# Kernel tuning notes

Measured on AMD Instinct MI355X. Metric: run time of the kernel, lower is better.

Reference implementation:

```python
import jax, jax.numpy as jnp
import numpy as np

B, S, D, H = 2, 2048, 1024, 16
HD = D // H  # head dim = 64


def setup_inputs() -> dict:
    key0 = jax.random.key(0)
    ks = jax.random.split(key0, 12)
    scale = 1.0 / np.sqrt(D)
    inp = {
        "query": jax.random.normal(ks[0], (B, S, D), jnp.float32),
        "key": jax.random.normal(ks[1], (B, S, D), jnp.float32),
        "value": jax.random.normal(ks[2], (B, S, D), jnp.float32),
        "mask": jax.random.randint(ks[3], (B, S), 0, 2, jnp.int32),
        "Wq": jax.random.normal(ks[4], (D, D), jnp.float32) * scale,
        "bq": jnp.zeros((D,), jnp.float32),
        "Wk": jax.random.normal(ks[5], (D, D), jnp.float32) * scale,
        "bk": jnp.zeros((D,), jnp.float32),
        "Wv": jax.random.normal(ks[6], (D, D), jnp.float32) * scale,
        "bv": jnp.zeros((D,), jnp.float32),
        "Wo": jax.random.normal(ks[7], (D, D), jnp.float32) * scale,
        "bo": jnp.zeros((D,), jnp.float32),
    }
    return inp


def _split_heads(x):  # (B,S,D) -> (B,H,S,HD)
    Bb, Ss, Dd = x.shape
    return x.reshape(Bb, Ss, H, HD).transpose(0, 2, 1, 3)


def reference(query, key, value, mask, Wq, bq, Wk, bk, Wv, bv, Wo, bo):
    # Linear projections (torch Linear: x @ W.T + b), split into heads.
    q = _split_heads(query @ Wq.T + bq)
    k = _split_heads(key @ Wk.T + bk)
    v = _split_heads(value @ Wv.T + bv)
    # Scaled dot-product scores: (B,H,S,S); NOTE: original divides by sqrt(head_dim).
    scores = jnp.einsum("bhqd,bhkd->bhqk", q, k) / np.sqrt(HD).astype(np.float32)
    # mask (B,S) masks KEY positions; broadcast over heads and query positions.
    scores = jnp.where(mask[:, None, None, :] == 0, jnp.float32(-1e9), scores)
    attn = jax.nn.softmax(scores, axis=-1)
    # Dropout is identity in eval mode.
    x = jnp.einsum("bhqk,bhkd->bhqd", attn, v)  # (B,H,S,HD)
    x = x.transpose(0, 2, 1, 3).reshape(query.shape[0], query.shape[1], D)
    return x @ Wo.T + bo
```

## Files before the change

### kernel.cpp

```cpp
#include <hip/hip_runtime.h>
#include <hip/hip_bf16.h>
#include <hip/hip_fp16.h>

#define BB 2
#define SS 2048
#define DD 1024
#define HH 16
#define HD 64
#define MM (BB * SS)

typedef __attribute__((ext_vector_type(8))) _Float16 half8;
typedef __attribute__((ext_vector_type(4))) float f32x4;
typedef __attribute__((ext_vector_type(4))) short short4v;

static __device__ __forceinline__ short f2h(float f) {
    _Float16 h = (_Float16)f;
    return __builtin_bit_cast(short, h);
}

static __device__ __forceinline__ unsigned pk2(float a, float b) {
    auto h = __builtin_amdgcn_cvt_pkrtz(a, b);
    return __builtin_bit_cast(unsigned, h);
}

static __device__ __forceinline__ float fexp2(float x) {
    return __builtin_amdgcn_exp2f(x);
}

static __device__ __forceinline__ void gload16(const void* g, void* l) {
    __builtin_amdgcn_global_load_lds(
        (const __attribute__((address_space(1))) unsigned*)g,
        (__attribute__((address_space(3))) unsigned*)l, 16, 0, 0);
}

__global__ __launch_bounds__(256) void cvt_kernel(
    const float* __restrict__ wq, const float* __restrict__ wk,
    const float* __restrict__ wv, const float* __restrict__ wo,
    const int* __restrict__ mask,
    short* __restrict__ wq16, short* __restrict__ wk16,
    short* __restrict__ wv16, short* __restrict__ wo16,
    float* __restrict__ mbias)
{
    const int i = (blockIdx.x * 256 + threadIdx.x) * 4;
    if (blockIdx.y == 4) {
        if (i >= BB * SS) return;
        const int4 mi = *(const int4*)&mask[i];
        float4 f;
        f.x = (mi.x == 0) ? -1.0e9f : 0.0f;
        f.y = (mi.y == 0) ? -1.0e9f : 0.0f;
        f.z = (mi.z == 0) ? -1.0e9f : 0.0f;
        f.w = (mi.w == 0) ? -1.0e9f : 0.0f;
        *(float4*)&mbias[i] = f;
        return;
    }
    const float* src; short* dst;
    switch (blockIdx.y) {
        case 0: src = wq; dst = wq16; break;
        case 1: src = wk; dst = wk16; break;
        case 2: src = wv; dst = wv16; break;
        default: src = wo; dst = wo16; break;
    }
    if (i >= DD * DD) return;
    const float4 f = *(const float4*)&src[i];
    short4v h;
    h.x = f2h(f.x); h.y = f2h(f.y); h.z = f2h(f.z); h.w = f2h(f.w);
    *(short4v*)&dst[i] = h;
}

template<bool AFP32>
__global__ __launch_bounds__(256) void gemm_f16(
    const void* __restrict__ A0, const void* __restrict__ A1, const void* __restrict__ A2,
    const short* __restrict__ W0, const short* __restrict__ W1, const short* __restrict__ W2,
    const float* __restrict__ b0, const float* __restrict__ b1, const float* __restrict__ b2,
    void* __restrict__ C0, void* __restrict__ C1, void* __restrict__ C2,
    int mode0, int mode1, int mode2)
{
    constexpr int TM = 64;
    constexpr int WN = 32;
    constexpr int NI = 2;

    const int z = blockIdx.z;
    const void* A = (z == 0) ? A0 : (z == 1) ? A1 : A2;
    const short* W = (z == 0) ? W0 : (z == 1) ? W1 : W2;
    const float* bias = (z == 0) ? b0 : (z == 1) ? b1 : b2;
    void* C = (z == 0) ? C0 : (z == 1) ? C1 : C2;
    const int mode = (z == 0) ? mode0 : (z == 1) ? mode1 : mode2;

    __shared__ short Asw[TM * 64];
    __shared__ short Bsw[128 * 64];

    const int t = threadIdx.x;
    const int wave = t >> 6, lane = t & 63;
    const int lr = lane & 15, lq = lane >> 4;
    const int wc = wave;
    const int m0 = blockIdx.x * TM, n0 = blockIdx.y * 128;
    const int K = DD;

    f32x4 acc[4][NI] = {};

    for (int k0 = 0; k0 < K; k0 += 64) {
        #pragma unroll
        for (int c = 0; c < 2; ++c) {
            const int b = c * 4096 + t * 16;
            const int row = b >> 7;
            const int coff = b & 127;
            if constexpr (AFP32) {
                const float* ap = (const float*)A +
                    (size_t)(m0 + row) * K + k0 + (coff >> 1);
                const float4 f0 = *(const float4*)ap;
                const float4 f1 = *(const float4*)(ap + 4);
                uint4 pv;
                pv.x = pk2(f0.x, f0.y);
                pv.y = pk2(f0.z, f0.w);
                pv.z = pk2(f1.x, f1.y);
                pv.w = pk2(f1.z, f1.w);
                *(uint4*)((char*)Asw + row * 128 + (coff ^ ((row & 7) << 4))) = pv;
            } else {
                const int scoff = coff ^ ((row & 7) << 4);
                gload16((const char*)A + ((size_t)(m0 + row) * K + k0) * 2 + scoff,
                        (char*)Asw + b);
            }
        }
        #pragma unroll
        for (int c = 0; c < 4; ++c) {
            const int b = c * 4096 + t * 16;
            const int row = b >> 7;
            const int coff = b & 127;
            const int scoff = coff ^ ((row & 7) << 4);
            gload16((const char*)W + ((size_t)(n0 + row) * K + k0) * 2 + scoff,
                    (char*)Bsw + b);
        }
        __syncthreads();

        half8 af[4][2], bf[NI][2];
        #pragma unroll
        for (int mi = 0; mi < 4; ++mi) {
            const int row = mi * 16 + lr;
            #pragma unroll
            for (int ks = 0; ks < 2; ++ks) {
                const int col = (ks * 32 + lq * 8) ^ ((row & 7) << 3);
                af[mi][ks] = *(const half8*)&Asw[row * 64 + col];
            }
        }
        #pragma unroll
        for (int ni = 0; ni < NI; ++ni) {
            const int row = wc * WN + ni * 16 + lr;
            #pragma unroll
            for (int ks = 0; ks < 2; ++ks) {
                const int col = (ks * 32 + lq * 8) ^ ((row & 7) << 3);
                bf[ni][ks] = *(const half8*)&Bsw[row * 64 + col];
            }
        }
        #pragma unroll
        for (int ks = 0; ks < 2; ++ks)
            #pragma unroll
            for (int mi = 0; mi < 4; ++mi)
                #pragma unroll
                for (int ni = 0; ni < NI; ++ni)
                    acc[mi][ni] = __builtin_amdgcn_mfma_f32_16x16x32_f16(
                        af[mi][ks], bf[ni][ks], acc[mi][ni], 0, 0, 0);
        __syncthreads();
    }

    if (mode == 2) {
        #pragma unroll
        for (int mi = 0; mi < 4; ++mi) {
            const int m = m0 + mi * 16 + lq * 4;
            const int bidx = m >> 11;
            const int s = m & (SS - 1);
            #pragma unroll
            for (int ni = 0; ni < NI; ++ni) {
                const int n = n0 + wc * WN + ni * 16 + lr;
                const int h = n >> 6, d = n & (HD - 1);
                const float bi = bias[n];
                short4v pv;
                pv.x = f2h(acc[mi][ni][0] + bi);
                pv.y = f2h(acc[mi][ni][1] + bi);
                pv.z = f2h(acc[mi][ni][2] + bi);
                pv.w = f2h(acc[mi][ni][3] + bi);
                *(short4v*)&((short*)C)[(((size_t)bidx * HH + h) * HD + d) * SS + s] = pv;
            }
        }
    } else {
        #pragma unroll
        for (int mi = 0; mi < 4; ++mi) {
            #pragma unroll
            for (int r = 0; r < 4; ++r) {
                const int m = m0 + mi * 16 + lq * 4 + r;
                const int bidx = m >> 11;
                const int s = m & (SS - 1);
                #pragma unroll
                for (int ni = 0; ni < NI; ++ni) {
                    const int n = n0 + wc * WN + ni * 16 + lr;
                    const float val = acc[mi][ni][r] + bias[n];
                    if (mode == 0) {
                        ((float*)C)[(size_t)m * DD + n] = val;
                    } else {
                        const int h = n >> 6, d = n & (HD - 1);
                        ((short*)C)[(((size_t)bidx * HH + h) * SS + s) * HD + d] = f2h(val);
                    }
                }
            }
        }
    }
}

static __device__ __forceinline__ void attn_tile_body(
    const short* __restrict__ Ks, const short* __restrict__ Vts,
    char* KsN, char* VtsN,
    const char* kb, const char* vb,
    int kv_stage, bool do_stage,
    const float* mrow, int kv0,
    const half8 qf[2], short* Pw,
    int t, int lr, int lq,
    f32x4 o[4], f32x4& ol, half8 ones8)
{
    const float SC2 = 0.18033688011112042f;

    if (do_stage) {
        #pragma unroll
        for (int c = 0; c < 2; ++c) {
            const int off = c * 4096 + t * 16;
            const int row = off >> 7, coff = off & 127;
            const int sw = coff ^ ((row & 7) << 4);
            gload16(kb + (size_t)(kv_stage + row) * 128 + sw, KsN + off);
            gload16(vb + (size_t)row * (SS * 2) + kv_stage * 2 + sw, VtsN + off);
        }
    }

    float4 mb[4];
    #pragma unroll
    for (int kt = 0; kt < 4; ++kt)
        mb[kt] = *(const float4*)&mrow[kv0 + kt * 16 + lq * 4];

    f32x4 sc[4] = {};
    __builtin_amdgcn_s_setprio(1);
    #pragma unroll
    for (int kt = 0; kt < 4; ++kt) {
        const int kr = kt * 16 + lr;
        #pragma unroll
        for (int ks = 0; ks < 2; ++ks) {
            half8 kf = *(const half8*)&Ks[kr * 64 + ((ks * 32 + lq * 8) ^ ((kr & 7) << 3))];
            sc[kt] = __builtin_amdgcn_mfma_f32_16x16x32_f16(kf, qf[ks], sc[kt], 0, 0, 0);
        }
    }
    __builtin_amdgcn_s_setprio(0);

    const int xsw = (lr & 7) << 3;
    #pragma unroll
    for (int kt = 0; kt < 4; ++kt) {
        const float p0 = fexp2(fmaf(sc[kt][0], SC2, mb[kt].x));
        const float p1 = fexp2(fmaf(sc[kt][1], SC2, mb[kt].y));
        const float p2 = fexp2(fmaf(sc[kt][2], SC2, mb[kt].z));
        const float p3 = fexp2(fmaf(sc[kt][3], SC2, mb[kt].w));
        const int cb = kt * 16 + lq * 4;
        uint2 pp;
        pp.x = pk2(p0, p1);
        pp.y = pk2(p2, p3);
        *(uint2*)&Pw[lr * 64 + (cb ^ xsw)] = pp;
    }

    half8 pf[2];
    #pragma unroll
    for (int ks = 0; ks < 2; ++ks)
        pf[ks] = *(const half8*)&Pw[lr * 64 + ((ks * 32 + lq * 8) ^ xsw)];
    __builtin_amdgcn_s_setprio(1);
    #pragma unroll
    for (int ks = 0; ks < 2; ++ks)
        ol = __builtin_amdgcn_mfma_f32_16x16x32_f16(pf[ks], ones8, ol, 0, 0, 0);
    #pragma unroll
    for (int dt = 0; dt < 4; ++dt) {
        const int dr = dt * 16 + lr;
        #pragma unroll
        for (int ks = 0; ks < 2; ++ks) {
            half8 vf = *(const half8*)&Vts[dr * 64 + ((ks * 32 + lq * 8) ^ ((dr & 7) << 3))];
            o[dt] = __builtin_amdgcn_mfma_f32_16x16x32_f16(pf[ks], vf, o[dt], 0, 0, 0);
        }
    }
    __builtin_amdgcn_s_setprio(0);

    __syncthreads();
}

__global__ __launch_bounds__(256) void attn_mfma_kernel(
    const short* __restrict__ q,
    const short* __restrict__ k,
    const short* __restrict__ vt,
    const float* __restrict__ mbias,
    short* __restrict__ x)
{
    const int lin = (blockIdx.z * HH + blockIdx.y) * (SS / 64) + blockIdx.x;
    const int swz = (lin & 7) * 128 + (lin >> 3);
    const int qt = swz & 31;
    const int hb = swz >> 5;
    const int h  = hb & (HH - 1);
    const int b  = hb >> 4;

    const int t = threadIdx.x;
    const int wave = t >> 6, lane = t & 63;
    const int lr = lane & 15;
    const int lq = lane >> 4;

    __shared__ short QPs[64 * 64];
    __shared__ short KsD[2][64 * 64];
    __shared__ short VtsD[2][64 * 64];

    const size_t base  = ((size_t)(b * HH + h)) * SS * HD;
    const size_t basev = ((size_t)(b * HH + h)) * HD * SS;
    const char* kb = (const char*)(k + base);
    const char* vb = (const char*)(vt + basev);

    {
        const char* qb = (const char*)(q + base + (size_t)qt * 64 * HD);
        #pragma unroll
        for (int c = 0; c < 2; ++c) {
            const int off = c * 4096 + t * 16;
            const int row = off >> 7, coff = off & 127;
            const int sw = coff ^ ((row & 7) << 4);
            gload16(qb + row * 128 + sw, (char*)QPs + off);
            gload16(kb + (size_t)row * 128 + sw, (char*)KsD[0] + off);
            gload16(vb + (size_t)row * (SS * 2) + sw, (char*)VtsD[0] + off);
        }
    }
    __syncthreads();

    half8 qf[2];
    #pragma unroll
    for (int ks = 0; ks < 2; ++ks) {
        const int r = wave * 16 + lr;
        qf[ks] = *(const half8*)&QPs[r * 64 + ((ks * 32 + lq * 8) ^ ((r & 7) << 3))];
    }
    __syncthreads();

    f32x4 o[4] = {};
    f32x4 ol = {};
    const float* mrow = &mbias[b * SS];
    short* Pw = &QPs[wave * 1024];

    const half8 ones8 = {1.0f16, 1.0f16, 1.0f16, 1.0f16,
                         1.0f16, 1.0f16, 1.0f16, 1.0f16};

    for (int kv0 = 0; kv0 < SS; kv0 += 128) {
        attn_tile_body(KsD[0], VtsD[0], (char*)KsD[1], (char*)VtsD[1],
                       kb, vb, kv0 + 64, true,
                       mrow, kv0, qf, Pw, t, lr, lq, o, ol, ones8);
        attn_tile_body(KsD[1], VtsD[1], (char*)KsD[0], (char*)VtsD[0],
                       kb, vb, kv0 + 128, (kv0 + 128) < SS,
                       mrow, kv0 + 64, qf, Pw, t, lr, lq, o, ol, ones8);
    }

    float linv[4];
    #pragma unroll
    for (int r = 0; r < 4; ++r) linv[r] = 1.0f / ol[r];
    const int srow = qt * 64 + wave * 16;
    #pragma unroll
    for (int dt = 0; dt < 4; ++dt)
        #pragma unroll
        for (int r = 0; r < 4; ++r)
            x[((size_t)b * SS + srow + lq * 4 + r) * DD + h * HD + dt * 16 + lr] =
                f2h(o[dt][r] * linv[r]);
}

extern "C" void kernel_launch(void* const* d_in, const int* in_sizes, int n_in,
                              void* d_out, int out_size, void* d_ws, size_t ws_size,
                              hipStream_t stream) {
    const float* query = (const float*)d_in[0];
    const float* key   = (const float*)d_in[1];
    const float* value = (const float*)d_in[2];
    const int*   mask  = (const int*)d_in[3];
    const float* Wq = (const float*)d_in[4];
    const float* bq = (const float*)d_in[5];
    const float* Wk = (const float*)d_in[6];
    const float* bk = (const float*)d_in[7];
    const float* Wv = (const float*)d_in[8];
    const float* bv = (const float*)d_in[9];
    const float* Wo = (const float*)d_in[10];
    const float* bo = (const float*)d_in[11];
    float* out = (float*)d_out;

    const size_t NACT = (size_t)MM * DD;
    const size_t NW   = (size_t)DD * DD;
    short* wq16  = (short*)d_ws;
    short* wk16  = wq16 + NW;
    short* wv16  = wk16 + NW;
    short* wo16  = wv16 + NW;
    short* q_ws  = wo16 + NW;
    short* k_ws  = q_ws + NACT;
    short* vt_ws = k_ws + NACT;
    float* mbias = (float*)(vt_ws + NACT);
    short* x16   = (short*)(mbias + BB * SS);

    cvt_kernel<<<dim3(NW / 4 / 256, 5), 256, 0, stream>>>(
        Wq, Wk, Wv, Wo, mask,
        wq16, wk16, wv16, wo16, mbias);

    gemm_f16<true><<<dim3(MM / 64, DD / 128, 3), 256, 0, stream>>>(
        query, key, value, wq16, wk16, wv16, bq, bk, bv,
        q_ws, k_ws, vt_ws, 1, 1, 2);

    attn_mfma_kernel<<<dim3(SS / 64, HH, BB), 256, 0, stream>>>(
        q_ws, k_ws, vt_ws, mbias, x16);

    gemm_f16<false><<<dim3(MM / 64, DD / 128, 1), 256, 0, stream>>>(
        x16, x16, x16, wo16, wo16, wo16, bo, bo, bo,
        out, out, out, 0, 0, 0);
}
```

Before: 131.8 us.

## Double-buffer GEMM LDS tiles to overlap global loads with MFMA

```diff
diff --git a/kernel.cpp b/kernel.cpp
--- a/kernel.cpp
+++ b/kernel.cpp
@@ -68,6 +68,98 @@
 }
 
 template<bool AFP32>
+static __device__ __forceinline__ void gemm_phase(
+    const short* __restrict__ AsCur, const short* __restrict__ BsCur,
+    char* AsNxt, char* BsNxt,
+    const void* __restrict__ A, const short* __restrict__ W,
+    int m0, int n0, int k_next, bool do_stage,
+    int t, int lr, int lq, int wc,
+    f32x4 acc[4][2])
+{
+    constexpr int WN = 32;
+    constexpr int NI = 2;
+    const int K = DD;
+
+    float4 af32[4];
+    if (do_stage) {
+        #pragma unroll
+        for (int c = 0; c < 4; ++c) {
+            const int b = c * 4096 + t * 16;
+            const int row = b >> 7;
+            const int coff = b & 127;
+            const int scoff = coff ^ ((row & 7) << 4);
+            gload16((const char*)W + ((size_t)(n0 + row) * K + k_next) * 2 + scoff,
+                    BsNxt + b);
+        }
+        #pragma unroll
+        for (int c = 0; c < 2; ++c) {
+            const int b = c * 4096 + t * 16;
+            const int row = b >> 7;
+            const int coff = b & 127;
+            if constexpr (AFP32) {
+                const float* ap = (const float*)A +
+                    (size_t)(m0 + row) * K + k_next + (coff >> 1);
+                af32[c * 2]     = *(const float4*)ap;
+                af32[c * 2 + 1] = *(const float4*)(ap + 4);
+            } else {
+                const int scoff = coff ^ ((row & 7) << 4);
+                gload16((const char*)A + ((size_t)(m0 + row) * K + k_next) * 2 + scoff,
+                        AsNxt + b);
+            }
+        }
+    }
+
+    half8 af[4][2], bf[NI][2];
+    #pragma unroll
+    for (int mi = 0; mi < 4; ++mi) {
+        const int row = mi * 16 + lr;
+        #pragma unroll
+        for (int ks = 0; ks < 2; ++ks) {
+            const int col = (ks * 32 + lq * 8) ^ ((row & 7) << 3);
+            af[mi][ks] = *(const half8*)&AsCur[row * 64 + col];
+        }
+    }
+    #pragma unroll
+    for (int ni = 0; ni < NI; ++ni) {
+        const int row = wc * WN + ni * 16 + lr;
+        #pragma unroll
+        for (int ks = 0; ks < 2; ++ks) {
+            const int col = (ks * 32 + lq * 8) ^ ((row & 7) << 3);
+            bf[ni][ks] = *(const half8*)&BsCur[row * 64 + col];
+        }
+    }
+    __builtin_amdgcn_s_setprio(1);
+    #pragma unroll
+    for (int ks = 0; ks < 2; ++ks)
+        #pragma unroll
+        for (int mi = 0; mi < 4; ++mi)
+            #pragma unroll
+            for (int ni = 0; ni < NI; ++ni)
+                acc[mi][ni] = __builtin_amdgcn_mfma_f32_16x16x32_f16(
+                    af[mi][ks], bf[ni][ks], acc[mi][ni], 0, 0, 0);
+    __builtin_amdgcn_s_setprio(0);
+
+    if (do_stage) {
+        if constexpr (AFP32) {
+            #pragma unroll
+            for (int c = 0; c < 2; ++c) {
+                const int b = c * 4096 + t * 16;
+                const int row = b >> 7;
+                const int coff = b & 127;
+                uint4 pv;
+                pv.x = pk2(af32[c * 2].x,     af32[c * 2].y);
+                pv.y = pk2(af32[c * 2].z,     af32[c * 2].w);
+                pv.z = pk2(af32[c * 2 + 1].x, af32[c * 2 + 1].y);
+                pv.w = pk2(af32[c * 2 + 1].z, af32[c * 2 + 1].w);
+                *(uint4*)(AsNxt + row * 128 + (coff ^ ((row & 7) << 4))) = pv;
+            }
+        }
+    }
+
+    __syncthreads();
+}
+
+template<bool AFP32>
 __global__ __launch_bounds__(256) void gemm_f16(
     const void* __restrict__ A0, const void* __restrict__ A1, const void* __restrict__ A2,
     const short* __restrict__ W0, const short* __restrict__ W1, const short* __restrict__ W2,
@@ -86,8 +178,8 @@
     void* C = (z == 0) ? C0 : (z == 1) ? C1 : C2;
     const int mode = (z == 0) ? mode0 : (z == 1) ? mode1 : mode2;
 
-    __shared__ short Asw[TM * 64];
-    __shared__ short Bsw[128 * 64];
+    __shared__ short Asw[2][TM * 64];
+    __shared__ short Bsw[2][128 * 64];
 
     const int t = threadIdx.x;
     const int wave = t >> 6, lane = t & 63;
@@ -98,15 +190,23 @@
 
     f32x4 acc[4][NI] = {};
 
-    for (int k0 = 0; k0 < K; k0 += 64) {
+    {
+        #pragma unroll
+        for (int c = 0; c < 4; ++c) {
+            const int b = c * 4096 + t * 16;
+            const int row = b >> 7;
+            const int coff = b & 127;
+            const int scoff = coff ^ ((row & 7) << 4);
+            gload16((const char*)W + ((size_t)(n0 + row) * K) * 2 + scoff,
+                    (char*)Bsw[0] + b);
+        }
         #pragma unroll
         for (int c = 0; c < 2; ++c) {
             const int b = c * 4096 + t * 16;
             const int row = b >> 7;
             const int coff = b & 127;
             if constexpr (AFP32) {
-                const float* ap = (const float*)A +
-                    (size_t)(m0 + row) * K + k0 + (coff >> 1);
+                const float* ap = (const float*)A + (size_t)(m0 + row) * K + (coff >> 1);
                 const float4 f0 = *(const float4*)ap;
                 const float4 f1 = *(const float4*)(ap + 4);
                 uint4 pv;
@@ -114,52 +214,23 @@
                 pv.y = pk2(f0.z, f0.w);
                 pv.z = pk2(f1.x, f1.y);
                 pv.w = pk2(f1.z, f1.w);
-                *(uint4*)((char*)Asw + row * 128 + (coff ^ ((row & 7) << 4))) = pv;
+                *(uint4*)((char*)Asw[0] + row * 128 + (coff ^ ((row & 7) << 4))) = pv;
             } else {
                 const int scoff = coff ^ ((row & 7) << 4);
-                gload16((const char*)A + ((size_t)(m0 + row) * K + k0) * 2 + scoff,
-                        (char*)Asw + b);
+                gload16((const char*)A + ((size_t)(m0 + row) * K) * 2 + scoff,
+                        (char*)Asw[0] + b);
             }
         }
-        #pragma unroll
-        for (int c = 0; c < 4; ++c) {
-            const int b = c * 4096 + t * 16;
-            const int row = b >> 7;
-            const int coff = b & 127;
-            const int scoff = coff ^ ((row & 7) << 4);
-            gload16((const char*)W + ((size_t)(n0 + row) * K + k0) * 2 + scoff,
-                    (char*)Bsw + b);
-        }
-        __syncthreads();
-
-        half8 af[4][2], bf[NI][2];
-        #pragma unroll
-        for (int mi = 0; mi < 4; ++mi) {
-            const int row = mi * 16 + lr;
-            #pragma unroll
-            for (int ks = 0; ks < 2; ++ks) {
-                const int col = (ks * 32 + lq * 8) ^ ((row & 7) << 3);
-                af[mi][ks] = *(const half8*)&Asw[row * 64 + col];
-            }
-        }
-        #pragma unroll
-        for (int ni = 0; ni < NI; ++ni) {
-            const int row = wc * WN + ni * 16 + lr;
-            #pragma unroll
-            for (int ks = 0; ks < 2; ++ks) {
-                const int col = (ks * 32 + lq * 8) ^ ((row & 7) << 3);
-                bf[ni][ks] = *(const half8*)&Bsw[row * 64 + col];
-            }
-        }
-        #pragma unroll
-        for (int ks = 0; ks < 2; ++ks)
-            #pragma unroll
-            for (int mi = 0; mi < 4; ++mi)
-                #pragma unroll
-                for (int ni = 0; ni < NI; ++ni)
-                    acc[mi][ni] = __builtin_amdgcn_mfma_f32_16x16x32_f16(
-                        af[mi][ks], bf[ni][ks], acc[mi][ni], 0, 0, 0);
-        __syncthreads();
+    }
+    __syncthreads();
+
+    for (int k0 = 0; k0 < K; k0 += 128) {
+        gemm_phase<AFP32>(Asw[0], Bsw[0], (char*)Asw[1], (char*)Bsw[1],
+                          A, W, m0, n0, k0 + 64, true,
+                          t, lr, lq, wc, acc);
+        gemm_phase<AFP32>(Asw[1], Bsw[1], (char*)Asw[0], (char*)Bsw[0],
+                          A, W, m0, n0, k0 + 128, (k0 + 128) < K,
+                          t, lr, lq, wc, acc);
     }
 
     if (mode == 2) {
```

Result: no change. 130.0 us (-1.3%).
